# Kernel tuning notes

Measured on AMD Instinct MI355X. Metric: run time of the kernel, lower is better.

## Reference

```python
import jax, jax.numpy as jnp
import numpy as np

N = 20000
E = 640000
H, C = 4, 64
L = 3
B = 16
EPS = 1e-5


def setup_inputs() -> dict:
    key = jax.random.key(0)
    ks = jax.random.split(key, 12)
    x = jax.random.normal(ks[0], (N, 256), dtype=jnp.float32)
    edge_index = jax.random.randint(ks[1], (2, E), 0, N, dtype=jnp.int64)
    batch = jnp.sort(jax.random.randint(ks[2], (N,), 0, B, dtype=jnp.int64))
    s = 0.05
    return {
        "x": x,
        "edge_index": edge_index,
        "batch": batch,
        "Wl": jax.random.normal(ks[3], (L, 256, H * C), dtype=jnp.float32) * s,
        "bl": jnp.zeros((L, H * C), dtype=jnp.float32),
        "Wr": jax.random.normal(ks[4], (L, 256, H * C), dtype=jnp.float32) * s,
        "br": jnp.zeros((L, H * C), dtype=jnp.float32),
        "att": jax.random.normal(ks[5], (L, H, C), dtype=jnp.float32) * s,
        "conv_bias": jnp.zeros((L, H * C), dtype=jnp.float32),
        "prelu_a": jnp.full((L,), 0.25, dtype=jnp.float32),
        "norm_w": jnp.ones((H * C,), dtype=jnp.float32),
        "norm_b": jnp.zeros((H * C,), dtype=jnp.float32),
        "norm_alpha": jnp.ones((H * C,), dtype=jnp.float32),
        "fc_W": jax.random.normal(ks[6], (H * C, 128), dtype=jnp.float32) * s,
        "fc_b": jnp.zeros((128,), dtype=jnp.float32),
    }


def graph_norm(h, w, b, alpha):
    # GraphNorm with batch=None: all rows form one segment (as in source forward)
    mean = jnp.mean(h, axis=0, keepdims=True)
    shifted = h - alpha * mean
    var = jnp.mean(shifted * shifted, axis=0, keepdims=True)
    return w * shifted / jnp.sqrt(var + EPS) + b


def gatv2_layer(h, src, dst, Wl, bl, Wr, br, att, bias):
    xl = (h @ Wl + bl).reshape(N, H, C)  # source transform
    xr = (h @ Wr + br).reshape(N, H, C)  # target transform
    m = jax.nn.leaky_relu(xl[src] + xr[dst], negative_slope=0.2)  # [Etot,H,C]
    e = jnp.einsum("ehc,hc->eh", m, att)  # [Etot,H]
    emax = jax.ops.segment_max(e, dst, num_segments=N)  # self-loops guarantee coverage
    ex = jnp.exp(e - emax[dst])
    denom = jax.ops.segment_sum(ex, dst, num_segments=N)
    alpha = ex / denom[dst]
    out = jax.ops.segment_sum(alpha[:, :, None] * xl[src], dst, num_segments=N)
    return out.reshape(N, H * C) + bias


def reference(x, edge_index, batch, Wl, bl, Wr, br, att, conv_bias, prelu_a,
              norm_w, norm_b, norm_alpha, fc_W, fc_b):
    loop = jnp.arange(N, dtype=edge_index.dtype)
    src = jnp.concatenate([edge_index[0], loop])  # add self-loops (PyG default)
    dst = jnp.concatenate([edge_index[1], loop])
    h = x
    for l in range(L):
        h = gatv2_layer(h, src, dst, Wl[l], bl[l], Wr[l], br[l], att[l], conv_bias[l])
        h = graph_norm(h, norm_w, norm_b, norm_alpha)
        h = jnp.where(h >= 0, h, prelu_a[l] * h)  # PReLU; dropout is identity in eval
    pooled = jax.ops.segment_sum(h, batch, num_segments=B)  # global_add_pool
    pooled = graph_norm(pooled, norm_w, norm_b, norm_alpha)  # shared norm reused after pool
    return pooled @ fc_W + fc_b
```

## Files before the change

### kernel.cpp

```cpp
#include <hip/hip_runtime.h>
#include <math.h>

#define N_NODES 20000
#define N_EDGES 640000
#define ETOT (N_EDGES + N_NODES)
#define HC 256
#define NLAYER 3
#define NBATCH 16
#define GEPS 1e-5f
#define NSLOT 64

typedef unsigned short u16;
typedef unsigned int u32;
typedef __attribute__((ext_vector_type(8))) short short8;
typedef __attribute__((ext_vector_type(4))) float floatx4;

__device__ __forceinline__ u16 f2bf(float f) {
    u32 u = __float_as_uint(f);
    u32 r = (u + 0x7FFFu + ((u >> 16) & 1u)) >> 16;
    return (u16)r;
}

__device__ __forceinline__ float4 bf2f4(uint2 u) {
    float4 r;
    r.x = __uint_as_float(u.x << 16);
    r.y = __uint_as_float(u.x & 0xFFFF0000u);
    r.z = __uint_as_float(u.y << 16);
    r.w = __uint_as_float(u.y & 0xFFFF0000u);
    return r;
}

__device__ __forceinline__ float dpp_red16(float x) {
    x += __int_as_float(__builtin_amdgcn_update_dpp(0, __float_as_int(x), 0xB1, 0xF, 0xF, true));
    x += __int_as_float(__builtin_amdgcn_update_dpp(0, __float_as_int(x), 0x4E, 0xF, 0xF, true));
    x += __int_as_float(__builtin_amdgcn_update_dpp(0, __float_as_int(x), 0x141, 0xF, 0xF, true));
    x += __int_as_float(__builtin_amdgcn_update_dpp(0, __float_as_int(x), 0x140, 0xF, 0xF, true));
    return x;
}


__global__ __launch_bounds__(256) void prep(const float* __restrict__ x, u16* __restrict__ xbf,
                                            const float* __restrict__ Wl, const float* __restrict__ Wr,
                                            u16* __restrict__ WT, uint4* __restrict__ zbase, int zq) {
    int b = blockIdx.x, tid = threadIdx.x;
    if (b < 1000) {
        for (int i = b * 256 + tid; i < 640000; i += 256000) {
            const float4* x4 = (const float4*)x + (size_t)i * 2;
            float4 a = x4[0], c = x4[1];
            u16 o[8] = {f2bf(a.x), f2bf(a.y), f2bf(a.z), f2bf(a.w),
                        f2bf(c.x), f2bf(c.y), f2bf(c.z), f2bf(c.w)};
            ((uint4*)xbf)[i] = *(const uint4*)o;
        }
    } else if (b < 1384) {
        __shared__ float T[32][33];
        int bi = b - 1000;
        int kb = bi & 7, nbk = (bi >> 3) & 15, l = bi >> 7;
        int n0 = nbk * 32, k0 = kb * 32;
        const float* W = ((n0 < 256) ? Wl : Wr) + (size_t)l * 65536;
        int nn = n0 & 255;
        int tx = tid & 31, ty = tid >> 5;
        #pragma unroll
        for (int i = 0; i < 4; ++i)
            T[ty + i * 8][tx] = W[(size_t)(k0 + ty + i * 8) * 256 + nn + tx];
        __syncthreads();
        u16* outw = WT + (size_t)l * 512 * 256;
        #pragma unroll
        for (int i = 0; i < 4; ++i)
            outw[(size_t)(n0 + ty + i * 8) * 256 + k0 + tx] = f2bf(T[tx][ty + i * 8]);
    } else {
        uint4 z = make_uint4(0, 0, 0, 0);
        for (int i = (b - 1384) * 256 + tid; i < zq; i += 120 * 256) zbase[i] = z;
    }
}


__global__ void count_deg(const int* __restrict__ dst, int* __restrict__ deg) {
    int e = blockIdx.x * 256 + threadIdx.x;
    if (e < N_EDGES) atomicAdd(&deg[dst[e]], 1);
}

__global__ __launch_bounds__(1024) void scan_excl(int* __restrict__ data, int* __restrict__ cursor) {
    __shared__ int wsum[16];
    int t = threadIdx.x, lane = t & 63, wid = t >> 6;
    int i0 = t * 20;
    int d[20];
    int tot = 0;
    #pragma unroll
    for (int j = 0; j < 20; ++j) {
        int i = i0 + j;
        int v = (i < N_NODES) ? (data[i] + 1) : 0;
        d[j] = v;
        tot += v;
    }
    int x = tot;
    #pragma unroll
    for (int off = 1; off < 64; off <<= 1) {
        int tmp = __shfl_up(x, off);
        if (lane >= off) x += tmp;
    }
    if (lane == 63) wsum[wid] = x;
    __syncthreads();
    if (t == 0) {
        int run = 0;
        #pragma unroll
        for (int w = 0; w < 16; ++w) { int tv = wsum[w]; wsum[w] = run; run += tv; }
    }
    __syncthreads();
    int run = wsum[wid] + x - tot;
    #pragma unroll
    for (int j = 0; j < 20; ++j) {
        int i = i0 + j;
        if (i < N_NODES) { data[i] = run; cursor[i] = run; }
        run += d[j];
    }
    if (t == 0) data[N_NODES] = ETOT;
}

__global__ void scatter_edges(const int* __restrict__ src, const int* __restrict__ dst,
                              int* __restrict__ cursor, int* __restrict__ col) {
    int t = blockIdx.x * 256 + threadIdx.x;
    if (t < N_NODES) {
        int p = atomicAdd(&cursor[t], 1);
        col[p] = t;
    } else if (t < N_NODES + N_EDGES) {
        int e = t - N_NODES;
        int p = atomicAdd(&cursor[dst[e]], 1);
        col[p] = src[e];
    }
}


__global__ __launch_bounds__(256) void gemm_mfma(
    const u16* __restrict__ Asrc, const float* __restrict__ slots_prev,
    const float* __restrict__ nw, const float* __restrict__ nb, const float* __restrict__ na,
    const float* __restrict__ pa, int prelu_idx, int use_norm,
    const u16* __restrict__ WT,
    const float* __restrict__ b0, const float* __restrict__ b1,
    u16* __restrict__ xlb, u16* __restrict__ xrb) {
    __shared__ u16 As[128][40];
    __shared__ u16 Bs[128][40];
    __shared__ float wcL[256], bbL[256];
    int row0 = blockIdx.x * 128;
    int nstrip = blockIdx.y;
    int ncol0 = nstrip * 128;
    const float* bias = (nstrip < 2) ? b0 : b1;
    u16* outp = (nstrip < 2) ? xlb : xrb;
    int c0 = (nstrip & 1) * 128;

    int tid = threadIdx.x;
    float ap = 0.f;
    if (use_norm) {
        int c = tid;
        float sum = 0.f, sq = 0.f;
        for (int s = 0; s < NSLOT; ++s) {
            sum += slots_prev[s * 512 + c];
            sq += slots_prev[s * 512 + 256 + c];
        }
        const float invn = 1.f / (float)N_NODES;
        float mean = sum * invn, Eh2 = sq * invn;
        float a = na[c];
        float var = Eh2 - (2.f * a - a * a) * mean * mean;
        float wc = nw[c] * rsqrtf(var + GEPS);
        wcL[c] = wc;
        bbL[c] = nb[c] - a * mean * wc;
        ap = pa[prelu_idx];
        __syncthreads();
    }

    int wave = tid >> 6, lane = tid & 63;
    int wm = (wave & 1) * 64, wn = (wave >> 1) * 64;
    int quad = lane >> 4, l16 = lane & 15;

    floatx4 acc[4][4] = {};

    int sr = tid >> 1;
    int sh = (tid & 1) * 16;

    for (int k0 = 0; k0 < 256; k0 += 32) {
        int gr = row0 + sr;
        uint4 av0 = make_uint4(0, 0, 0, 0), av1 = make_uint4(0, 0, 0, 0);
        if (gr < N_NODES) {
            const u16* p = Asrc + (size_t)gr * 256 + k0 + sh;
            av0 = *(const uint4*)p;
            av1 = *(const uint4*)(p + 8);
        }
        if (use_norm) {
            int kb2 = k0 + sh;
            u16 tmp[16];
            *(uint4*)tmp = av0;
            *(uint4*)(tmp + 8) = av1;
            float4 wv0 = *(const float4*)&wcL[kb2], wv1 = *(const float4*)&wcL[kb2 + 4];
            float4 wv2 = *(const float4*)&wcL[kb2 + 8], wv3 = *(const float4*)&wcL[kb2 + 12];
            float4 bv0 = *(const float4*)&bbL[kb2], bv1 = *(const float4*)&bbL[kb2 + 4];
            float4 bv2 = *(const float4*)&bbL[kb2 + 8], bv3 = *(const float4*)&bbL[kb2 + 12];
            float wvf[16] = {wv0.x, wv0.y, wv0.z, wv0.w, wv1.x, wv1.y, wv1.z, wv1.w,
                             wv2.x, wv2.y, wv2.z, wv2.w, wv3.x, wv3.y, wv3.z, wv3.w};
            float bvf[16] = {bv0.x, bv0.y, bv0.z, bv0.w, bv1.x, bv1.y, bv1.z, bv1.w,
                             bv2.x, bv2.y, bv2.z, bv2.w, bv3.x, bv3.y, bv3.z, bv3.w};
            u16 outv[16];
            #pragma unroll
            for (int j = 0; j < 16; ++j) {
                float vv = __uint_as_float(((u32)tmp[j]) << 16);
                float t2 = vv * wvf[j] + bvf[j];
                t2 = fmaxf(t2, ap * t2);
                outv[j] = f2bf(t2);
            }
            av0 = *(const uint4*)outv;
            av1 = *(const uint4*)(outv + 8);
        }
        const u16* q = WT + (size_t)(ncol0 + sr) * 256 + k0 + sh;
        uint4 bw0 = *(const uint4*)q;
        uint4 bw1 = *(const uint4*)(q + 8);
        *(uint4*)&As[sr][sh] = av0;
        *(uint4*)&As[sr][sh + 8] = av1;
        *(uint4*)&Bs[sr][sh] = bw0;
        *(uint4*)&Bs[sr][sh + 8] = bw1;
        __syncthreads();

        short8 af[4], bfr[4];
        #pragma unroll
        for (int mi = 0; mi < 4; ++mi)
            af[mi] = *(const short8*)&As[wm + mi * 16 + l16][quad * 8];
        #pragma unroll
        for (int ni = 0; ni < 4; ++ni)
            bfr[ni] = *(const short8*)&Bs[wn + ni * 16 + l16][quad * 8];
        #pragma unroll
        for (int mi = 0; mi < 4; ++mi)
            #pragma unroll
            for (int ni = 0; ni < 4; ++ni)
                acc[mi][ni] = __builtin_amdgcn_mfma_f32_16x16x32_bf16(af[mi], bfr[ni], acc[mi][ni], 0, 0, 0);
        __syncthreads();
    }

    #pragma unroll
    for (int ni = 0; ni < 4; ++ni) {
        int col = c0 + wn + ni * 16 + l16;
        float bv = bias[col];
        #pragma unroll
        for (int mi = 0; mi < 4; ++mi) {
            int gr = row0 + wm + mi * 16 + quad * 4;
            #pragma unroll
            for (int r = 0; r < 4; ++r) {
                if (gr + r < N_NODES)
                    outp[(size_t)(gr + r) * 256 + col] = f2bf(acc[mi][ni][r] + bv);
            }
        }
    }
}


__device__ __forceinline__ void gat_load8(const int* __restrict__ col, int j, int lane,
                                          const u16* __restrict__ xlb, uint2 (&rr)[8]) {
    int cv = col[j + (lane & 7)];
    #pragma unroll
    for (int u = 0; u < 8; ++u) {
        int s = __builtin_amdgcn_readlane(cv, u);
        rr[u] = *((const uint2*)(xlb + ((size_t)(u32)s << 8)) + lane);
    }
}

__device__ __forceinline__ void gat_comp8(const uint2 (&rr)[8], const float4& xrv, const float4& attv,
                                          float& denom, float4& acc) {
    #pragma unroll
    for (int u = 0; u < 8; ++u) {
        float4 a = bf2f4(rr[u]);
        float vx = a.x + xrv.x, vy = a.y + xrv.y;
        float vz = a.z + xrv.z, vw = a.w + xrv.w;
        vx = fmaxf(vx, 0.2f * vx);
        vy = fmaxf(vy, 0.2f * vy);
        vz = fmaxf(vz, 0.2f * vz);
        vw = fmaxf(vw, 0.2f * vw);
        float p = vx * attv.x + vy * attv.y + vz * attv.z + vw * attv.w;
        p = dpp_red16(p);
        float w = exp2f(p);
        denom += w;
        acc.x += w * a.x; acc.y += w * a.y;
        acc.z += w * a.z; acc.w += w * a.w;
    }
}

__global__ __launch_bounds__(256) void gat_agg(
    const u16* __restrict__ xlb, const u16* __restrict__ xrb,
    const int* __restrict__ rowptr, const int* __restrict__ col,
    const float* __restrict__ att_l, const float* __restrict__ bias_l,
    u16* __restrict__ hB, float* __restrict__ slot) {
    __shared__ float sred[4][520];
    int wid = threadIdx.x >> 6, lane = threadIdx.x & 63;
    int node = blockIdx.x * 4 + wid;
    const float LOG2E = 1.4426950408889634f;
    float4 attv = ((const float4*)att_l)[lane];
    attv.x *= LOG2E; attv.y *= LOG2E; attv.z *= LOG2E; attv.w *= LOG2E;
    float4 xrv = bf2f4(((const uint2*)xrb)[(size_t)node * 64 + lane]);
    int beg = __builtin_amdgcn_readfirstlane(rowptr[node]);
    int end = __builtin_amdgcn_readfirstlane(rowptr[node + 1]);

    float denom = 0.f;
    float4 acc = make_float4(0.f, 0.f, 0.f, 0.f);

    int nb = (end - beg) >> 3;
    int j = beg;
    uint2 rA[8], rB[8];
    if (nb > 0) gat_load8(col, j, lane, xlb, rA);
    int b = 0;
    while (b < nb) {
        if (b + 1 < nb) gat_load8(col, j + 8, lane, xlb, rB);
        gat_comp8(rA, xrv, attv, denom, acc);
        ++b; j += 8;
        if (b < nb) {
            if (b + 1 < nb) gat_load8(col, j + 8, lane, xlb, rA);
            gat_comp8(rB, xrv, attv, denom, acc);
            ++b; j += 8;
        }
    }
    for (; j < end; ++j) {
        int s = __builtin_amdgcn_readfirstlane(col[j]);
        uint2 r = *((const uint2*)(xlb + ((size_t)(u32)s << 8)) + lane);
        float4 a = bf2f4(r);
        float vx = a.x + xrv.x, vy = a.y + xrv.y;
        float vz = a.z + xrv.z, vw = a.w + xrv.w;
        vx = fmaxf(vx, 0.2f * vx);
        vy = fmaxf(vy, 0.2f * vy);
        vz = fmaxf(vz, 0.2f * vz);
        vw = fmaxf(vw, 0.2f * vw);
        float p = vx * attv.x + vy * attv.y + vz * attv.z + vw * attv.w;
        p = dpp_red16(p);
        float w = exp2f(p);
        denom += w;
        acc.x += w * a.x; acc.y += w * a.y; acc.z += w * a.z; acc.w += w * a.w;
    }

    float inv = 1.f / denom;
    float4 b4 = ((const float4*)bias_l)[lane];
    float4 o;
    o.x = acc.x * inv + b4.x; o.y = acc.y * inv + b4.y;
    o.z = acc.z * inv + b4.z; o.w = acc.w * inv + b4.w;
    u16 ob[4] = {f2bf(o.x), f2bf(o.y), f2bf(o.z), f2bf(o.w)};
    ((uint2*)hB)[(size_t)node * 64 + lane] = *(const uint2*)ob;

    int cb2 = lane * 4;
    sred[wid][cb2 + 0] = o.x; sred[wid][cb2 + 1] = o.y;
    sred[wid][cb2 + 2] = o.z; sred[wid][cb2 + 3] = o.w;
    sred[wid][256 + cb2 + 0] = o.x * o.x; sred[wid][256 + cb2 + 1] = o.y * o.y;
    sred[wid][256 + cb2 + 2] = o.z * o.z; sred[wid][256 + cb2 + 3] = o.w * o.w;
    __syncthreads();
    int t = threadIdx.x;
    #pragma unroll
    for (int h = 0; h < 2; ++h) {
        int idx = t + h * 256;
        float s = sred[0][idx] + sred[1][idx] + sred[2][idx] + sred[3][idx];
        atomicAdd(&slot[(blockIdx.x & (NSLOT - 1)) * 512 + idx], s);
    }
}


__global__ __launch_bounds__(256) void pool_kernel(const u16* __restrict__ hB,
                                                   const int* __restrict__ batch,
                                                   const float* __restrict__ slots2,
                                                   const float* __restrict__ nw, const float* __restrict__ nb,
                                                   const float* __restrict__ na, const float* __restrict__ pa,
                                                   float* __restrict__ pooled) {
    __shared__ float accs[NBATCH][256];
    int c = threadIdx.x;
    float sum = 0.f, sq = 0.f;
    for (int s = 0; s < NSLOT; ++s) {
        sum += slots2[s * 512 + c];
        sq += slots2[s * 512 + 256 + c];
    }
    const float invn = 1.f / (float)N_NODES;
    float mean = sum * invn, Eh2 = sq * invn;
    float a = na[c];
    float var = Eh2 - (2.f * a - a * a) * mean * mean;
    float wc = nw[c] * rsqrtf(var + GEPS);
    float bb = nb[c] - a * mean * wc;
    float ap = pa[2];

    #pragma unroll
    for (int b = 0; b < NBATCH; ++b) accs[b][c] = 0.f;
    int r0 = blockIdx.x * 100;
    int r1 = min(N_NODES, r0 + 100);
    for (int i = r0; i < r1; ++i) {
        float v = __uint_as_float(((u32)hB[(size_t)i * 256 + c]) << 16);
        v = v * wc + bb;
        v = fmaxf(v, ap * v);
        accs[batch[i]][c] += v;
    }
    int bmin = batch[r0], bmax = batch[r1 - 1];
    for (int b = bmin; b <= bmax; ++b) atomicAdd(&pooled[b * 256 + c], accs[b][c]);
}


__global__ __launch_bounds__(256) void pool_norm(const float* __restrict__ pooled,
                                                 const float* __restrict__ nw, const float* __restrict__ nb,
                                                 const float* __restrict__ na,
                                                 float* __restrict__ pn) {
    int c = threadIdx.x;
    float mean = 0.f, sq = 0.f;
    #pragma unroll
    for (int i = 0; i < NBATCH; ++i) {
        float v = pooled[i * 256 + c];
        mean += v; sq += v * v;
    }
    mean *= (1.f / NBATCH); sq *= (1.f / NBATCH);
    float a = na[c];
    float var = sq - (2.f * a - a * a) * mean * mean;
    float wc = nw[c] * rsqrtf(var + GEPS);
    float bb = nb[c] - a * mean * wc;
    #pragma unroll
    for (int i = 0; i < NBATCH; ++i)
        pn[i * 256 + c] = pooled[i * 256 + c] * wc + bb;
}


__global__ __launch_bounds__(256) void fc_kernel(const float* __restrict__ pn,
                                                 const float* __restrict__ fcW, const float* __restrict__ fcb,
                                                 float* __restrict__ out) {
    __shared__ float pnl[256];
    __shared__ float part[128];
    int b = blockIdx.x;
    int t = threadIdx.x;
    pnl[t] = pn[b * 256 + t];
    __syncthreads();
    int o = t & 127, half = t >> 7;
    float s = 0.f;
    int kbase = half * 128;
    #pragma unroll 8
    for (int k = 0; k < 128; ++k)
        s += pnl[kbase + k] * fcW[(kbase + k) * 128 + o];
    if (half == 1) part[o] = s;
    __syncthreads();
    if (half == 0) out[b * 128 + o] = s + part[o] + fcb[o];
}


extern "C" void kernel_launch(void* const* d_in, const int* in_sizes, int n_in,
                              void* d_out, int out_size, void* d_ws, size_t ws_size,
                              hipStream_t stream) {
    const float* x    = (const float*)d_in[0];
    const int*   ei   = (const int*)d_in[1];
    const int*   batch= (const int*)d_in[2];
    const float* Wl   = (const float*)d_in[3];
    const float* bl   = (const float*)d_in[4];
    const float* Wr   = (const float*)d_in[5];
    const float* br   = (const float*)d_in[6];
    const float* att  = (const float*)d_in[7];
    const float* cb   = (const float*)d_in[8];
    const float* pa   = (const float*)d_in[9];
    const float* nw   = (const float*)d_in[10];
    const float* nb   = (const float*)d_in[11];
    const float* na   = (const float*)d_in[12];
    const float* fcW  = (const float*)d_in[13];
    const float* fcb  = (const float*)d_in[14];
    float* out = (float*)d_out;

    char* ws = (char*)d_ws;
    size_t off = 0;
    auto carve = [&](size_t bytes) -> void* {
        void* p = (void*)(ws + off);
        off += (bytes + 255) & ~(size_t)255;
        return p;
    };
    size_t z0 = off;
    int*   rowptr = (int*)carve((N_NODES + 1) * sizeof(int));
    float* slots  = (float*)carve((size_t)NLAYER * NSLOT * 512 * sizeof(float));
    float* pooled = (float*)carve(NBATCH * HC * sizeof(float));
    size_t z1 = off;
    int*   cursor = (int*)carve(N_NODES * sizeof(int));
    int*   colidx = (int*)carve((size_t)ETOT * sizeof(int));
    u16*   xlb    = (u16*)carve((size_t)N_NODES * HC * sizeof(u16));
    u16*   xrb    = (u16*)carve((size_t)N_NODES * HC * sizeof(u16));
    u16*   hB     = (u16*)carve((size_t)N_NODES * HC * sizeof(u16));
    u16*   xbf    = (u16*)carve((size_t)N_NODES * HC * sizeof(u16));
    u16*   WT     = (u16*)carve((size_t)NLAYER * 512 * 256 * sizeof(u16));
    float* pn     = (float*)carve(NBATCH * HC * sizeof(float));

    int zq = (int)((z1 - z0) / 16);
    const int* srcp = ei;
    const int* dstp = ei + N_EDGES;

    prep<<<1504, 256, 0, stream>>>(x, xbf, Wl, Wr, WT, (uint4*)(ws + z0), zq);
    count_deg<<<(N_EDGES + 255) / 256, 256, 0, stream>>>(dstp, rowptr);
    scan_excl<<<1, 1024, 0, stream>>>(rowptr, cursor);
    scatter_edges<<<(ETOT + 255) / 256, 256, 0, stream>>>(srcp, dstp, cursor, colidx);

    for (int l = 0; l < NLAYER; ++l) {
        const u16* Asrc = (l == 0) ? xbf : hB;
        const float* slots_prev = slots + (size_t)((l > 0) ? (l - 1) : 0) * NSLOT * 512;
        gemm_mfma<<<dim3(157, 4), 256, 0, stream>>>(Asrc, slots_prev, nw, nb, na, pa,
                                                    (l > 0) ? (l - 1) : 0, (l > 0) ? 1 : 0,
                                                    WT + (size_t)l * 512 * 256,
                                                    bl + l * 256, br + l * 256, xlb, xrb);
        gat_agg<<<5000, 256, 0, stream>>>(xlb, xrb, rowptr, colidx, att + l * 256, cb + l * 256,
                                          hB, slots + (size_t)l * NSLOT * 512);
    }
    pool_kernel<<<200, 256, 0, stream>>>(hB, batch, slots + (size_t)2 * NSLOT * 512,
                                         nw, nb, na, pa, pooled);
    pool_norm<<<1, 256, 0, stream>>>(pooled, nw, nb, na, pn);
    fc_kernel<<<NBATCH, 256, 0, stream>>>(pn, fcW, fcb, out);
}
```

Baseline: 490.1 us.

## Process two destination nodes per wavefront in GAT aggregation; fuse pool norm into FC

Each wavefront in the GAT aggregation kernel now handles two destination nodes and interleaves their 8-edge gather batches. This doubles the number of independent memory loads in flight per wave, to hide gather latency, and halves the number of blocks and slot atomics. The cost is roughly doubled register use for the load buffers, which may lower occupancy, and a serial tail for whichever node has more edges. Separately, the pooled-graph normalization is folded into the FC kernel, which removes one tiny launch and its intermediate buffer.

```diff
diff --git a/kernel.cpp b/kernel.cpp
--- a/kernel.cpp
+++ b/kernel.cpp
@@ -259,23 +259,51 @@
     }
 }
 
+__device__ __forceinline__ void gat_edge1(uint2 r, const float4& xrv, const float4& attv,
+                                          float& denom, float4& acc) {
+    float4 a = bf2f4(r);
+    float vx = a.x + xrv.x, vy = a.y + xrv.y;
+    float vz = a.z + xrv.z, vw = a.w + xrv.w;
+    vx = fmaxf(vx, 0.2f * vx);
+    vy = fmaxf(vy, 0.2f * vy);
+    vz = fmaxf(vz, 0.2f * vz);
+    vw = fmaxf(vw, 0.2f * vw);
+    float p = vx * attv.x + vy * attv.y + vz * attv.z + vw * attv.w;
+    p = dpp_red16(p);
+    float w = exp2f(p);
+    denom += w;
+    acc.x += w * a.x; acc.y += w * a.y;
+    acc.z += w * a.z; acc.w += w * a.w;
+}
+
 __device__ __forceinline__ void gat_comp8(const uint2 (&rr)[8], const float4& xrv, const float4& attv,
                                           float& denom, float4& acc) {
     #pragma unroll
-    for (int u = 0; u < 8; ++u) {
-        float4 a = bf2f4(rr[u]);
-        float vx = a.x + xrv.x, vy = a.y + xrv.y;
-        float vz = a.z + xrv.z, vw = a.w + xrv.w;
-        vx = fmaxf(vx, 0.2f * vx);
-        vy = fmaxf(vy, 0.2f * vy);
-        vz = fmaxf(vz, 0.2f * vz);
-        vw = fmaxf(vw, 0.2f * vw);
-        float p = vx * attv.x + vy * attv.y + vz * attv.z + vw * attv.w;
-        p = dpp_red16(p);
-        float w = exp2f(p);
-        denom += w;
-        acc.x += w * a.x; acc.y += w * a.y;
-        acc.z += w * a.z; acc.w += w * a.w;
+    for (int u = 0; u < 8; ++u) gat_edge1(rr[u], xrv, attv, denom, acc);
+}
+
+__device__ __forceinline__ void gat_tail(const int* __restrict__ col, const u16* __restrict__ xlb,
+                                         int lane, int j, int end,
+                                         const float4& xrv, const float4& attv,
+                                         float& denom, float4& acc) {
+    int nb = (end - j) >> 3;
+    uint2 tA[8], tB[8];
+    if (nb > 0) gat_load8(col, j, lane, xlb, tA);
+    int b = 0;
+    while (b < nb) {
+        if (b + 1 < nb) gat_load8(col, j + 8, lane, xlb, tB);
+        gat_comp8(tA, xrv, attv, denom, acc);
+        ++b; j += 8;
+        if (b < nb) {
+            if (b + 1 < nb) gat_load8(col, j + 8, lane, xlb, tA);
+            gat_comp8(tB, xrv, attv, denom, acc);
+            ++b; j += 8;
+        }
+    }
+    for (; j < end; ++j) {
+        int s = __builtin_amdgcn_readfirstlane(col[j]);
+        uint2 r = *((const uint2*)(xlb + ((size_t)(u32)s << 8)) + lane);
+        gat_edge1(r, xrv, attv, denom, acc);
     }
 }
 
@@ -284,70 +312,82 @@
     const int* __restrict__ rowptr, const int* __restrict__ col,
     const float* __restrict__ att_l, const float* __restrict__ bias_l,
     u16* __restrict__ hB, float* __restrict__ slot) {
-    __shared__ float sred[4][520];
+    __shared__ float sred[8][520];
     int wid = threadIdx.x >> 6, lane = threadIdx.x & 63;
-    int node = blockIdx.x * 4 + wid;
+    int nodeA = blockIdx.x * 8 + wid * 2;
+    int nodeB = nodeA + 1;
     const float LOG2E = 1.4426950408889634f;
     float4 attv = ((const float4*)att_l)[lane];
     attv.x *= LOG2E; attv.y *= LOG2E; attv.z *= LOG2E; attv.w *= LOG2E;
-    float4 xrv = bf2f4(((const uint2*)xrb)[(size_t)node * 64 + lane]);
-    int beg = __builtin_amdgcn_readfirstlane(rowptr[node]);
-    int end = __builtin_amdgcn_readfirstlane(rowptr[node + 1]);
-
-    float denom = 0.f;
-    float4 acc = make_float4(0.f, 0.f, 0.f, 0.f);
-
-    int nb = (end - beg) >> 3;
-    int j = beg;
-    uint2 rA[8], rB[8];
-    if (nb > 0) gat_load8(col, j, lane, xlb, rA);
+    float4 xrvA = bf2f4(((const uint2*)xrb)[(size_t)nodeA * 64 + lane]);
+    float4 xrvB = bf2f4(((const uint2*)xrb)[(size_t)nodeB * 64 + lane]);
+    int begA = __builtin_amdgcn_readfirstlane(rowptr[nodeA]);
+    int endA = __builtin_amdgcn_readfirstlane(rowptr[nodeA + 1]);
+    int begB = endA;
+    int endB = __builtin_amdgcn_readfirstlane(rowptr[nodeA + 2]);
+
+    float denomA = 0.f, denomB = 0.f;
+    float4 accA = make_float4(0.f, 0.f, 0.f, 0.f);
+    float4 accB = make_float4(0.f, 0.f, 0.f, 0.f);
+
+    int nbA = (endA - begA) >> 3, nbB = (endB - begB) >> 3;
+    int m = nbA < nbB ? nbA : nbB;
+    int jA = begA, jB = begB;
+
+    uint2 rA0[8], rA1[8], rB0[8], rB1[8];
+    if (m > 0) { gat_load8(col, jA, lane, xlb, rA0); gat_load8(col, jB, lane, xlb, rB0); }
     int b = 0;
-    while (b < nb) {
-        if (b + 1 < nb) gat_load8(col, j + 8, lane, xlb, rB);
-        gat_comp8(rA, xrv, attv, denom, acc);
-        ++b; j += 8;
-        if (b < nb) {
-            if (b + 1 < nb) gat_load8(col, j + 8, lane, xlb, rA);
-            gat_comp8(rB, xrv, attv, denom, acc);
-            ++b; j += 8;
-        }
-    }
-    for (; j < end; ++j) {
-        int s = __builtin_amdgcn_readfirstlane(col[j]);
-        uint2 r = *((const uint2*)(xlb + ((size_t)(u32)s << 8)) + lane);
-        float4 a = bf2f4(r);
-        float vx = a.x + xrv.x, vy = a.y + xrv.y;
-        float vz = a.z + xrv.z, vw = a.w + xrv.w;
-        vx = fmaxf(vx, 0.2f * vx);
-        vy = fmaxf(vy, 0.2f * vy);
-        vz = fmaxf(vz, 0.2f * vz);
-        vw = fmaxf(vw, 0.2f * vw);
-        float p = vx * attv.x + vy * attv.y + vz * attv.z + vw * attv.w;
-        p = dpp_red16(p);
-        float w = exp2f(p);
-        denom += w;
-        acc.x += w * a.x; acc.y += w * a.y; acc.z += w * a.z; acc.w += w * a.w;
-    }
-
-    float inv = 1.f / denom;
+    while (b < m) {
+        if (b + 1 < m) { gat_load8(col, jA + 8, lane, xlb, rA1); gat_load8(col, jB + 8, lane, xlb, rB1); }
+        gat_comp8(rA0, xrvA, attv, denomA, accA);
+        gat_comp8(rB0, xrvB, attv, denomB, accB);
+        ++b; jA += 8; jB += 8;
+        if (b < m) {
+            if (b + 1 < m) { gat_load8(col, jA + 8, lane, xlb, rA0); gat_load8(col, jB + 8, lane, xlb, rB0); }
+            gat_comp8(rA1, xrvA, attv, denomA, accA);
+            gat_comp8(rB1, xrvB, attv, denomB, accB);
+            ++b; jA += 8; jB += 8;
+        }
+    }
+    gat_tail(col, xlb, lane, jA, endA, xrvA, attv, denomA, accA);
+    gat_tail(col, xlb, lane, jB, endB, xrvB, attv, denomB, accB);
+
     float4 b4 = ((const float4*)bias_l)[lane];
-    float4 o;
-    o.x = acc.x * inv + b4.x; o.y = acc.y * inv + b4.y;
-    o.z = acc.z * inv + b4.z; o.w = acc.w * inv + b4.w;
-    u16 ob[4] = {f2bf(o.x), f2bf(o.y), f2bf(o.z), f2bf(o.w)};
-    ((uint2*)hB)[(size_t)node * 64 + lane] = *(const uint2*)ob;
-
     int cb2 = lane * 4;
-    sred[wid][cb2 + 0] = o.x; sred[wid][cb2 + 1] = o.y;
-    sred[wid][cb2 + 2] = o.z; sred[wid][cb2 + 3] = o.w;
-    sred[wid][256 + cb2 + 0] = o.x * o.x; sred[wid][256 + cb2 + 1] = o.y * o.y;
-    sred[wid][256 + cb2 + 2] = o.z * o.z; sred[wid][256 + cb2 + 3] = o.w * o.w;
+
+    {
+        float inv = 1.f / denomA;
+        float4 o;
+        o.x = accA.x * inv + b4.x; o.y = accA.y * inv + b4.y;
+        o.z = accA.z * inv + b4.z; o.w = accA.w * inv + b4.w;
+        u16 ob[4] = {f2bf(o.x), f2bf(o.y), f2bf(o.z), f2bf(o.w)};
+        ((uint2*)hB)[(size_t)nodeA * 64 + lane] = *(const uint2*)ob;
+        int s0 = wid * 2;
+        sred[s0][cb2 + 0] = o.x; sred[s0][cb2 + 1] = o.y;
+        sred[s0][cb2 + 2] = o.z; sred[s0][cb2 + 3] = o.w;
+        sred[s0][256 + cb2 + 0] = o.x * o.x; sred[s0][256 + cb2 + 1] = o.y * o.y;
+        sred[s0][256 + cb2 + 2] = o.z * o.z; sred[s0][256 + cb2 + 3] = o.w * o.w;
+    }
+    {
+        float inv = 1.f / denomB;
+        float4 o;
+        o.x = accB.x * inv + b4.x; o.y = accB.y * inv + b4.y;
+        o.z = accB.z * inv + b4.z; o.w = accB.w * inv + b4.w;
+        u16 ob[4] = {f2bf(o.x), f2bf(o.y), f2bf(o.z), f2bf(o.w)};
+        ((uint2*)hB)[(size_t)nodeB * 64 + lane] = *(const uint2*)ob;
+        int s1 = wid * 2 + 1;
+        sred[s1][cb2 + 0] = o.x; sred[s1][cb2 + 1] = o.y;
+        sred[s1][cb2 + 2] = o.z; sred[s1][cb2 + 3] = o.w;
+        sred[s1][256 + cb2 + 0] = o.x * o.x; sred[s1][256 + cb2 + 1] = o.y * o.y;
+        sred[s1][256 + cb2 + 2] = o.z * o.z; sred[s1][256 + cb2 + 3] = o.w * o.w;
+    }
     __syncthreads();
     int t = threadIdx.x;
     #pragma unroll
     for (int h = 0; h < 2; ++h) {
         int idx = t + h * 256;
-        float s = sred[0][idx] + sred[1][idx] + sred[2][idx] + sred[3][idx];
+        float s = sred[0][idx] + sred[1][idx] + sred[2][idx] + sred[3][idx]
+                + sred[4][idx] + sred[5][idx] + sred[6][idx] + sred[7][idx];
         atomicAdd(&slot[(blockIdx.x & (NSLOT - 1)) * 512 + idx], s);
     }
 }
@@ -389,36 +429,27 @@
 }
 
 
-__global__ __launch_bounds__(256) void pool_norm(const float* __restrict__ pooled,
+__global__ __launch_bounds__(256) void fc_kernel(const float* __restrict__ pooled,
                                                  const float* __restrict__ nw, const float* __restrict__ nb,
                                                  const float* __restrict__ na,
-                                                 float* __restrict__ pn) {
-    int c = threadIdx.x;
-    float mean = 0.f, sq = 0.f;
-    #pragma unroll
-    for (int i = 0; i < NBATCH; ++i) {
-        float v = pooled[i * 256 + c];
-        mean += v; sq += v * v;
-    }
-    mean *= (1.f / NBATCH); sq *= (1.f / NBATCH);
-    float a = na[c];
-    float var = sq - (2.f * a - a * a) * mean * mean;
-    float wc = nw[c] * rsqrtf(var + GEPS);
-    float bb = nb[c] - a * mean * wc;
-    #pragma unroll
-    for (int i = 0; i < NBATCH; ++i)
-        pn[i * 256 + c] = pooled[i * 256 + c] * wc + bb;
-}
-
-
-__global__ __launch_bounds__(256) void fc_kernel(const float* __restrict__ pn,
                                                  const float* __restrict__ fcW, const float* __restrict__ fcb,
                                                  float* __restrict__ out) {
     __shared__ float pnl[256];
     __shared__ float part[128];
     int b = blockIdx.x;
     int t = threadIdx.x;
-    pnl[t] = pn[b * 256 + t];
+    float mean = 0.f, sq = 0.f;
+    #pragma unroll
+    for (int i = 0; i < NBATCH; ++i) {
+        float v = pooled[i * 256 + t];
+        mean += v; sq += v * v;
+    }
+    mean *= (1.f / NBATCH); sq *= (1.f / NBATCH);
+    float a = na[t];
+    float var = sq - (2.f * a - a * a) * mean * mean;
+    float wc = nw[t] * rsqrtf(var + GEPS);
+    float bb = nb[t] - a * mean * wc;
+    pnl[t] = pooled[b * 256 + t] * wc + bb;
     __syncthreads();
     int o = t & 127, half = t >> 7;
     float s = 0.f;
@@ -471,7 +502,6 @@
     u16*   hB     = (u16*)carve((size_t)N_NODES * HC * sizeof(u16));
     u16*   xbf    = (u16*)carve((size_t)N_NODES * HC * sizeof(u16));
     u16*   WT     = (u16*)carve((size_t)NLAYER * 512 * 256 * sizeof(u16));
-    float* pn     = (float*)carve(NBATCH * HC * sizeof(float));
 
     int zq = (int)((z1 - z0) / 16);
     const int* srcp = ei;
@@ -489,11 +519,10 @@
                                                     (l > 0) ? (l - 1) : 0, (l > 0) ? 1 : 0,
                                                     WT + (size_t)l * 512 * 256,
                                                     bl + l * 256, br + l * 256, xlb, xrb);
-        gat_agg<<<5000, 256, 0, stream>>>(xlb, xrb, rowptr, colidx, att + l * 256, cb + l * 256,
+        gat_agg<<<2500, 256, 0, stream>>>(xlb, xrb, rowptr, colidx, att + l * 256, cb + l * 256,
                                           hB, slots + (size_t)l * NSLOT * 512);
     }
     pool_kernel<<<200, 256, 0, stream>>>(hB, batch, slots + (size_t)2 * NSLOT * 512,
                                          nw, nb, na, pa, pooled);
-    pool_norm<<<1, 256, 0, stream>>>(pooled, nw, nb, na, pn);
-    fc_kernel<<<NBATCH, 256, 0, stream>>>(pn, fcW, fcb, out);
-}
+    fc_kernel<<<NBATCH, 256, 0, stream>>>(pooled, nw, nb, na, fcW, fcb, out);
+}
```

New measurement: 533.7 us. 1.09x slower.

## Prefetch next GEMM k-tile into registers and fuse pool norm into FC

Applied to the files above, without the earlier changes.

The MFMA GEMM loop now issues global loads for the next k-tile into registers before running the current tile's MFMAs, then writes them to shared memory after a barrier. This software pipelining is meant to hide global load latency behind matrix math. It costs extra registers and an additional barrier per iteration. Separately, the pooled GraphNorm is computed inside each FC block, which removes one kernel launch at the price of each block redundantly recomputing the per-column statistics.

```diff
diff --git a/kernel.cpp b/kernel.cpp
--- a/kernel.cpp
+++ b/kernel.cpp
@@ -175,48 +175,48 @@
 
     int sr = tid >> 1;
     int sh = (tid & 1) * 16;
-
-    for (int k0 = 0; k0 < 256; k0 += 32) {
-        int gr = row0 + sr;
-        uint4 av0 = make_uint4(0, 0, 0, 0), av1 = make_uint4(0, 0, 0, 0);
-        if (gr < N_NODES) {
-            const u16* p = Asrc + (size_t)gr * 256 + k0 + sh;
-            av0 = *(const uint4*)p;
-            av1 = *(const uint4*)(p + 8);
+    bool arow_ok = (row0 + sr) < N_NODES;
+    const u16* Abase = Asrc + (size_t)(row0 + sr) * 256 + sh;
+    const u16* Bbase = WT + (size_t)(ncol0 + sr) * 256 + sh;
+
+    uint4 a0, a1, bw0, bw1;
+    uint4 na0, na1, nb0, nb1;
+
+    auto stage = [&](int k0, uint4& x0, uint4& x1, uint4& y0, uint4& y1) {
+        x0 = make_uint4(0, 0, 0, 0);
+        x1 = make_uint4(0, 0, 0, 0);
+        if (arow_ok) {
+            x0 = *(const uint4*)(Abase + k0);
+            x1 = *(const uint4*)(Abase + k0 + 8);
         }
+        y0 = *(const uint4*)(Bbase + k0);
+        y1 = *(const uint4*)(Bbase + k0 + 8);
+    };
+
+    auto writeAB = [&](int k0, uint4 x0, uint4 x1, uint4 y0, uint4 y1) {
         if (use_norm) {
             int kb2 = k0 + sh;
             u16 tmp[16];
-            *(uint4*)tmp = av0;
-            *(uint4*)(tmp + 8) = av1;
-            float4 wv0 = *(const float4*)&wcL[kb2], wv1 = *(const float4*)&wcL[kb2 + 4];
-            float4 wv2 = *(const float4*)&wcL[kb2 + 8], wv3 = *(const float4*)&wcL[kb2 + 12];
-            float4 bv0 = *(const float4*)&bbL[kb2], bv1 = *(const float4*)&bbL[kb2 + 4];
-            float4 bv2 = *(const float4*)&bbL[kb2 + 8], bv3 = *(const float4*)&bbL[kb2 + 12];
-            float wvf[16] = {wv0.x, wv0.y, wv0.z, wv0.w, wv1.x, wv1.y, wv1.z, wv1.w,
-                             wv2.x, wv2.y, wv2.z, wv2.w, wv3.x, wv3.y, wv3.z, wv3.w};
-            float bvf[16] = {bv0.x, bv0.y, bv0.z, bv0.w, bv1.x, bv1.y, bv1.z, bv1.w,
-                             bv2.x, bv2.y, bv2.z, bv2.w, bv3.x, bv3.y, bv3.z, bv3.w};
+            *(uint4*)tmp = x0;
+            *(uint4*)(tmp + 8) = x1;
             u16 outv[16];
             #pragma unroll
             for (int j = 0; j < 16; ++j) {
                 float vv = __uint_as_float(((u32)tmp[j]) << 16);
-                float t2 = vv * wvf[j] + bvf[j];
+                float t2 = vv * wcL[kb2 + j] + bbL[kb2 + j];
                 t2 = fmaxf(t2, ap * t2);
                 outv[j] = f2bf(t2);
             }
-            av0 = *(const uint4*)outv;
-            av1 = *(const uint4*)(outv + 8);
+            x0 = *(const uint4*)outv;
+            x1 = *(const uint4*)(outv + 8);
         }
-        const u16* q = WT + (size_t)(ncol0 + sr) * 256 + k0 + sh;
-        uint4 bw0 = *(const uint4*)q;
-        uint4 bw1 = *(const uint4*)(q + 8);
-        *(uint4*)&As[sr][sh] = av0;
-        *(uint4*)&As[sr][sh + 8] = av1;
-        *(uint4*)&Bs[sr][sh] = bw0;
-        *(uint4*)&Bs[sr][sh + 8] = bw1;
-        __syncthreads();
-
+        *(uint4*)&As[sr][sh] = x0;
+        *(uint4*)&As[sr][sh + 8] = x1;
+        *(uint4*)&Bs[sr][sh] = y0;
+        *(uint4*)&Bs[sr][sh + 8] = y1;
+    };
+
+    auto mfma_tile = [&]() {
         short8 af[4], bfr[4];
         #pragma unroll
         for (int mi = 0; mi < 4; ++mi)
@@ -229,8 +229,20 @@
             #pragma unroll
             for (int ni = 0; ni < 4; ++ni)
                 acc[mi][ni] = __builtin_amdgcn_mfma_f32_16x16x32_bf16(af[mi], bfr[ni], acc[mi][ni], 0, 0, 0);
+    };
+
+    stage(0, a0, a1, bw0, bw1);
+    writeAB(0, a0, a1, bw0, bw1);
+    __syncthreads();
+
+    for (int k0 = 32; k0 < 256; k0 += 32) {
+        stage(k0, na0, na1, nb0, nb1);
+        mfma_tile();
         __syncthreads();
-    }
+        writeAB(k0, na0, na1, nb0, nb1);
+        __syncthreads();
+    }
+    mfma_tile();
 
     #pragma unroll
     for (int ni = 0; ni < 4; ++ni) {
@@ -389,36 +401,27 @@
 }
 
 
-__global__ __launch_bounds__(256) void pool_norm(const float* __restrict__ pooled,
+__global__ __launch_bounds__(256) void fc_kernel(const float* __restrict__ pooled,
                                                  const float* __restrict__ nw, const float* __restrict__ nb,
                                                  const float* __restrict__ na,
-                                                 float* __restrict__ pn) {
-    int c = threadIdx.x;
-    float mean = 0.f, sq = 0.f;
-    #pragma unroll
-    for (int i = 0; i < NBATCH; ++i) {
-        float v = pooled[i * 256 + c];
-        mean += v; sq += v * v;
-    }
-    mean *= (1.f / NBATCH); sq *= (1.f / NBATCH);
-    float a = na[c];
-    float var = sq - (2.f * a - a * a) * mean * mean;
-    float wc = nw[c] * rsqrtf(var + GEPS);
-    float bb = nb[c] - a * mean * wc;
-    #pragma unroll
-    for (int i = 0; i < NBATCH; ++i)
-        pn[i * 256 + c] = pooled[i * 256 + c] * wc + bb;
-}
-
-
-__global__ __launch_bounds__(256) void fc_kernel(const float* __restrict__ pn,
                                                  const float* __restrict__ fcW, const float* __restrict__ fcb,
                                                  float* __restrict__ out) {
     __shared__ float pnl[256];
     __shared__ float part[128];
     int b = blockIdx.x;
     int t = threadIdx.x;
-    pnl[t] = pn[b * 256 + t];
+    float mean = 0.f, sq = 0.f;
+    #pragma unroll
+    for (int i = 0; i < NBATCH; ++i) {
+        float v = pooled[i * 256 + t];
+        mean += v; sq += v * v;
+    }
+    mean *= (1.f / NBATCH); sq *= (1.f / NBATCH);
+    float a = na[t];
+    float var = sq - (2.f * a - a * a) * mean * mean;
+    float wc = nw[t] * rsqrtf(var + GEPS);
+    float bb = nb[t] - a * mean * wc;
+    pnl[t] = pooled[b * 256 + t] * wc + bb;
     __syncthreads();
     int o = t & 127, half = t >> 7;
     float s = 0.f;
@@ -471,7 +474,6 @@
     u16*   hB     = (u16*)carve((size_t)N_NODES * HC * sizeof(u16));
     u16*   xbf    = (u16*)carve((size_t)N_NODES * HC * sizeof(u16));
     u16*   WT     = (u16*)carve((size_t)NLAYER * 512 * 256 * sizeof(u16));
-    float* pn     = (float*)carve(NBATCH * HC * sizeof(float));
 
     int zq = (int)((z1 - z0) / 16);
     const int* srcp = ei;
@@ -494,6 +496,5 @@
     }
     pool_kernel<<<200, 256, 0, stream>>>(hB, batch, slots + (size_t)2 * NSLOT * 512,
                                          nw, nb, na, pa, pooled);
-    pool_norm<<<1, 256, 0, stream>>>(pooled, nw, nb, na, pn);
-    fc_kernel<<<NBATCH, 256, 0, stream>>>(pn, fcW, fcb, out);
-}
+    fc_kernel<<<NBATCH, 256, 0, stream>>>(pooled, nw, nb, na, fcW, fcb, out);
+}
```

After: 519.7 us. +6.0%, slower.
